# Kernel tuning notes

Hardware: AMD Instinct MI355X
Metric: run time of the kernel (lower is better)

Reference implementation:

```python
import jax, jax.numpy as jnp
import numpy as np

B, S, HID = 2, 1024, 4096
NH, NKV, HD = 32, 8, 128
GROUPS = NH // NKV  # 4
BITS = 8
SCALING = HD ** -0.5


def quantize_lastdim(x, bits=BITS):
    """Asymmetric min-max fake-quant per row of the last dim (groupsize=-1),
    matching ActQuantizer.find_params + quantize/dequantize."""
    qmax = float(2 ** bits - 1)
    xmin = jnp.minimum(jnp.min(x, axis=-1, keepdims=True), 0.0)
    xmax = jnp.maximum(jnp.max(x, axis=-1, keepdims=True), 0.0)
    rng = xmax - xmin
    scale = jnp.where(rng == 0, 1.0, rng / qmax)
    zero = jnp.round(-xmin / scale)
    q = jnp.clip(jnp.round(x / scale) + zero, 0.0, qmax)
    return (q - zero) * scale


def rotate_half(x):
    x1, x2 = jnp.split(x, 2, axis=-1)
    return jnp.concatenate([-x2, x1], axis=-1)


def setup_inputs() -> dict:
    key = jax.random.key(0)
    ks = jax.random.split(key, 5)
    hidden_states = jax.random.normal(ks[0], (B, S, HID), dtype=jnp.float32)
    w_std = 0.02
    Wq = w_std * jax.random.normal(ks[1], (NH * HD, HID), dtype=jnp.float32)
    Wk = w_std * jax.random.normal(ks[2], (NKV * HD, HID), dtype=jnp.float32)
    Wv = w_std * jax.random.normal(ks[3], (NKV * HD, HID), dtype=jnp.float32)
    Wo = w_std * jax.random.normal(ks[4], (HID, NH * HD), dtype=jnp.float32)
    # RoPE tables (theta=10000)
    inv_freq = 1.0 / (10000.0 ** (jnp.arange(0, HD, 2, dtype=jnp.float32) / HD))
    freqs = jnp.outer(jnp.arange(S, dtype=jnp.float32), inv_freq)  # [S, HD/2]
    emb = jnp.concatenate([freqs, freqs], axis=-1)  # [S, HD]
    cos = jnp.broadcast_to(jnp.cos(emb)[None], (B, S, HD)).astype(jnp.float32)
    sin = jnp.broadcast_to(jnp.sin(emb)[None], (B, S, HD)).astype(jnp.float32)
    # additive causal mask [B,1,S,S]
    causal = jnp.tril(jnp.ones((S, S), dtype=bool))
    attention_mask = jnp.where(causal, 0.0, -1e9).astype(jnp.float32)
    attention_mask = jnp.broadcast_to(attention_mask[None, None], (B, 1, S, S))
    return {"hidden_states": hidden_states, "cos": cos, "sin": sin,
            "attention_mask": attention_mask, "Wq": Wq, "Wk": Wk, "Wv": Wv, "Wo": Wo}


def reference(hidden_states, cos, sin, attention_mask, Wq, Wk, Wv, Wo):
    b, s, _ = hidden_states.shape
    # projections -> [B, H, S, D]
    q = (hidden_states @ Wq.T).reshape(b, s, NH, HD).transpose(0, 2, 1, 3)
    k = (hidden_states @ Wk.T).reshape(b, s, NKV, HD).transpose(0, 2, 1, 3)
    v = (hidden_states @ Wv.T).reshape(b, s, NKV, HD).transpose(0, 2, 1, 3)
    # RoPE (HF: unsqueeze cos/sin at head dim)
    c = cos[:, None, :, :]
    si = sin[:, None, :, :]
    q = q * c + rotate_half(q) * si
    k = k * c + rotate_half(k) * si
    # SmoothK per-channel: subtract per-channel mean over the sequence
    # (softmax-invariant outlier smoothing of K before quantization)
    k = k - jnp.mean(k, axis=2, keepdims=True)
    # activation fake-quant of Q, K (per token over head_dim)
    q = quantize_lastdim(q)
    k = quantize_lastdim(k)
    # V quantized along the sequence axis (module transposes dims 2,3 first)
    v = quantize_lastdim(v.transpose(0, 1, 3, 2)).transpose(0, 1, 3, 2)
    # GQA repeat
    k_rep = jnp.repeat(k, GROUPS, axis=1)
    v_rep = jnp.repeat(v, GROUPS, axis=1)
    scores = jnp.einsum('bhqd,bhkd->bhqk', q, k_rep) * SCALING + attention_mask
    w = jax.nn.softmax(scores.astype(jnp.float32), axis=-1).astype(q.dtype)
    # fake-quant attention weights per row (groupsize=-1, so no padding)
    w = quantize_lastdim(w)
    attn = jnp.einsum('bhqk,bhkd->bhqd', w, v_rep)
    attn = attn.transpose(0, 2, 1, 3).reshape(b, s, NH * HD)
    out = attn @ Wo.T
    return (out, w)
```

## Files before the change

kernel.cpp:

```cpp
#include <hip/hip_runtime.h>
#include <math.h>
#include <stdint.h>

typedef unsigned int u32;
typedef unsigned short u16;
typedef __bf16 bf16x8 __attribute__((ext_vector_type(8)));
typedef float f32x4 __attribute__((ext_vector_type(4)));
typedef unsigned short u16x8 __attribute__((ext_vector_type(8)));
typedef unsigned short u16x4 __attribute__((ext_vector_type(4)));

constexpr int   Bb  = 2;
constexpr int   Ss  = 1024;
constexpr int   HID = 4096;
constexpr int   NH  = 32;
constexpr int   NKV = 8;
constexpr int   HD  = 128;
constexpr float SCALING = 0.0883883476483184405501f;

enum { M_QKV = 0, M_OUT = 3 };

__device__ __forceinline__ u16 f2bf(float f) {
  u32 u = __builtin_bit_cast(u32, f);
  u = u + 0x7fffu + ((u >> 16) & 1u);
  return (u16)(u >> 16);
}

__device__ __forceinline__ void gld_lds16(const void* g, void* l) {
  __builtin_amdgcn_global_load_lds(
      (const __attribute__((address_space(1))) u32*)(uintptr_t)g,
      (__attribute__((address_space(3))) u32*)(uintptr_t)l, 16, 0, 0);
}

template <int MODE>
__global__ __launch_bounds__(512) void mfma_gemm(
    const u16* __restrict__ Abf_g,
    const u16* __restrict__ B0, const u16* __restrict__ B1,
    const u16* __restrict__ B2,
    float* __restrict__ Cf, float* __restrict__ Ck, float* __restrict__ Cv,
    int K) {
  __shared__ u16 As[3][128 * 64];
  __shared__ u16 Bs[3][256 * 64];

  const int tid = threadIdx.x;
  const int lane = tid & 63;
  const int wid = tid >> 6;
  const int wr = wid >> 2;
  const int wc = wid & 3;
  const int fr = lane & 15;
  const int fq = lane >> 4;

  const int m0 = blockIdx.y * 128;
  int nloc = 0;

  const u16* Abf = Abf_g + (size_t)m0 * K;
  const u16* Bp = nullptr;
  int which = 0;

  if (MODE == M_QKV) {
    const int j = blockIdx.x;
    if (j < 16)      { which = 0; Bp = B0 + (size_t)j * 256 * K;        nloc = j * 256; }
    else if (j < 20) { which = 1; Bp = B1 + (size_t)(j - 16) * 256 * K; nloc = (j - 16) * 256; }
    else             { which = 2; Bp = B2 + (size_t)(j - 20) * 256 * K; nloc = (j - 20) * 256; }
  } else {
    Bp = B0 + (size_t)blockIdx.x * 256 * K;
    nloc = blockIdx.x * 256;
  }

  f32x4 acc[4][4];
#pragma unroll
  for (int i = 0; i < 4; i++)
#pragma unroll
    for (int j = 0; j < 4; j++) acc[i][j] = (f32x4){0.f, 0.f, 0.f, 0.f};

  const int arow0 = wr * 64 + wc * 16;
  const int brow0 = wc * 64 + wr * 32;
  const int sub8 = lane >> 3;
  const int sl8 = lane & 7;

  auto stageA = [&](int t, int s) {
    const int ko = t * 64;
#pragma unroll
    for (int g = 0; g < 2; ++g) {
      const int r0 = arow0 + g * 8;
      const int row = r0 + sub8;
      gld_lds16(Abf + (size_t)row * K + ko + ((sl8 ^ (row & 7)) * 8),
                &As[s][r0 * 64]);
    }
  };
  auto stageB2 = [&](int t, int s, int gbase) {
    const int ko = t * 64;
#pragma unroll
    for (int g = 0; g < 2; ++g) {
      const int r0 = brow0 + (gbase + g) * 8;
      const int row = r0 + sub8;
      gld_lds16(Bp + (size_t)row * K + ko + ((sl8 ^ (row & 7)) * 8),
                &Bs[s][r0 * 64]);
    }
  };

  const int nk = K >> 6;

  stageA(0, 0); stageB2(0, 0, 0); stageB2(0, 0, 2);
  stageA(1, 1); stageB2(1, 1, 0); stageB2(1, 1, 2);
  asm volatile("s_waitcnt vmcnt(6)" ::: "memory");
  __builtin_amdgcn_sched_barrier(0);
  __builtin_amdgcn_s_barrier();

  int buf = 0, nxt = 2;
  for (int kt = 0; kt < nk; ++kt) {
    const bool st = (kt + 2 < nk);

    {
      bf16x8 av[4], bv[4];
#pragma unroll
      for (int i = 0; i < 4; ++i) {
        const int r = wr * 64 + i * 16 + fr;
        av[i] = *(const bf16x8*)&As[buf][r * 64 + ((fq ^ (r & 7)) * 8)];
      }
#pragma unroll
      for (int j = 0; j < 4; ++j) {
        const int r = wc * 64 + j * 16 + fr;
        bv[j] = *(const bf16x8*)&Bs[buf][r * 64 + ((fq ^ (r & 7)) * 8)];
      }
      if (st) { stageA(kt + 2, nxt); stageB2(kt + 2, nxt, 0); }
      __builtin_amdgcn_s_barrier();
      asm volatile("s_waitcnt lgkmcnt(0)" ::: "memory");
      __builtin_amdgcn_sched_barrier(0);
      __builtin_amdgcn_s_setprio(1);
#pragma unroll
      for (int i = 0; i < 4; i++)
#pragma unroll
        for (int j = 0; j < 4; j++)
          acc[i][j] = __builtin_amdgcn_mfma_f32_16x16x32_bf16(av[i], bv[j], acc[i][j], 0, 0, 0);
      __builtin_amdgcn_s_setprio(0);
    }

    {
      bf16x8 av[4], bv[4];
#pragma unroll
      for (int i = 0; i < 4; ++i) {
        const int r = wr * 64 + i * 16 + fr;
        av[i] = *(const bf16x8*)&As[buf][r * 64 + (((4 + fq) ^ (r & 7)) * 8)];
      }
#pragma unroll
      for (int j = 0; j < 4; ++j) {
        const int r = wc * 64 + j * 16 + fr;
        bv[j] = *(const bf16x8*)&Bs[buf][r * 64 + (((4 + fq) ^ (r & 7)) * 8)];
      }
      if (st) { stageB2(kt + 2, nxt, 2); }
      __builtin_amdgcn_s_barrier();
      asm volatile("s_waitcnt lgkmcnt(0)" ::: "memory");
      __builtin_amdgcn_sched_barrier(0);
      __builtin_amdgcn_s_setprio(1);
#pragma unroll
      for (int i = 0; i < 4; i++)
#pragma unroll
        for (int j = 0; j < 4; j++)
          acc[i][j] = __builtin_amdgcn_mfma_f32_16x16x32_bf16(av[i], bv[j], acc[i][j], 0, 0, 0);
      __builtin_amdgcn_s_setprio(0);
    }

    if (st) {
      asm volatile("s_waitcnt vmcnt(6)" ::: "memory");
    } else {
      asm volatile("s_waitcnt vmcnt(0)" ::: "memory");
    }
    __builtin_amdgcn_sched_barrier(0);
    __builtin_amdgcn_s_barrier();
    buf = (buf == 2) ? 0 : buf + 1;
    nxt = (nxt == 2) ? 0 : nxt + 1;
  }

#pragma unroll
  for (int i = 0; i < 4; i++) {
#pragma unroll
    for (int j = 0; j < 4; j++) {
      const int n = nloc + wc * 64 + j * 16 + fr;
#pragma unroll
      for (int e = 0; e < 4; e++) {
        const int m = m0 + wr * 64 + i * 16 + fq * 4 + e;
        float val = acc[i][j][e];
        if (MODE == M_QKV) {
          const int b = m >> 10, s = m & 1023, h = n >> 7, d = n & 127;
          if (which == 0)      Cf[((size_t)(b * NH + h) * Ss + s) * HD + d] = val;
          else if (which == 1) Ck[((size_t)(b * NKV + h) * Ss + s) * HD + d] = val;
          else                 Cv[((size_t)(b * NKV + h) * HD + d) * Ss + s] = val;
        } else {
          Cf[(size_t)m * HID + n] = val;
        }
      }
    }
  }
}

__global__ __launch_bounds__(256) void fused_attn(
    const u16* __restrict__ qb,
    const u16* __restrict__ kb,
    const u16* __restrict__ vTb,
    float* __restrict__ wout,
    u16* __restrict__ attnb) {
  __shared__ u16 Ks[64 * 128];
  __shared__ u16 Vs[128 * 64];
  __shared__ u16 plds[4][16 * 64];
  __shared__ float scl_l[4][16];

  const int a = 15 - (int)(blockIdx.x >> 6);
  const int bh = blockIdx.x & 63;
  const int b = bh >> 5, h = bh & 31;
  const int kv = h >> 2;
  const int tid = threadIdx.x;
  const int lane = tid & 63;
  const int wq = tid >> 6;
  const int fr = lane & 15, fq = lane >> 4;

  const int nt = a + 1;
  const int Q0 = a * 64;
  const int qw0 = Q0 + wq * 16;

  const u16* Kb = kb + (size_t)(b * NKV + kv) * Ss * HD;
  const u16* Vb = vTb + (size_t)(b * NKV + kv) * HD * Ss;
  float* wrow = wout + (size_t)bh * Ss * Ss;

  if (a < 15) {
    const int base = 64 * nt;
    const int n4 = 16 * (15 - a);
#pragma unroll
    for (int r0 = 0; r0 < 4; ++r0) {
      const int row = Q0 + r0 * 16 + (tid >> 4);
      float4* wp = (float4*)&wrow[(size_t)row * Ss + base];
      for (int c = tid & 15; c < n4; c += 16) wp[c] = float4{0.f, 0.f, 0.f, 0.f};
    }
  }

  bf16x8 qf[4];
#pragma unroll
  for (int kk = 0; kk < 4; kk++)
    qf[kk] = *(const bf16x8*)&qb[((size_t)bh * Ss + qw0 + fr) * HD + kk * 32 + fq * 8];

  float m[4], l[4];
#pragma unroll
  for (int i = 0; i < 4; i++) { m[i] = -1e30f; l[i] = 0.f; }

  for (int t = 0; t < nt; ++t) {
    __syncthreads();
#pragma unroll
    for (int c = 0; c < 4; ++c) {
      const int idx0 = (c * 4 + wq) * 64;
      const int idx = idx0 + lane;
      const int row = idx >> 4, sl = idx & 15;
      const int slot = sl ^ (row & 15);
      gld_lds16(Kb + (size_t)(t * 64 + row) * HD + slot * 8, &Ks[idx0 * 8]);
    }
    __syncthreads();

    f32x4 sa[4];
#pragma unroll
    for (int jn = 0; jn < 4; jn++) sa[jn] = (f32x4){0.f, 0.f, 0.f, 0.f};
#pragma unroll
    for (int kk = 0; kk < 4; ++kk) {
      bf16x8 kfv[4];
#pragma unroll
      for (int jn = 0; jn < 4; ++jn) {
        const int row = jn * 16 + fr;
        kfv[jn] = *(const bf16x8*)&Ks[row * 128 + (((kk * 4 + fq) ^ fr) * 8)];
      }
#pragma unroll
      for (int jn = 0; jn < 4; ++jn)
        sa[jn] = __builtin_amdgcn_mfma_f32_16x16x32_bf16(qf[kk], kfv[jn], sa[jn], 0, 0, 0);
    }

    const bool diag = (t == a);
#pragma unroll
    for (int e = 0; e < 4; ++e) {
      const int qrow = qw0 + fq * 4 + e;
      float sv[4];
      float rmax = -1e30f;
#pragma unroll
      for (int jn = 0; jn < 4; ++jn) {
        float s = sa[jn][e] * SCALING;
        if (diag && (t * 64 + jn * 16 + fr > qrow)) s = -1e30f;
        sv[jn] = s;
        rmax = fmaxf(rmax, s);
      }
#pragma unroll
      for (int o = 1; o < 16; o <<= 1) rmax = fmaxf(rmax, __shfl_xor(rmax, o));
      const float mn = fmaxf(m[e], rmax);
      const float cc = __expf(m[e] - mn);
      float rs = __expf(sv[0] - mn) + __expf(sv[1] - mn) +
                 __expf(sv[2] - mn) + __expf(sv[3] - mn);
#pragma unroll
      for (int o = 1; o < 16; o <<= 1) rs += __shfl_xor(rs, o);
      l[e] = l[e] * cc + rs;
      m[e] = mn;
    }
  }

  float scl[4];
#pragma unroll
  for (int e = 0; e < 4; e++) scl[e] = 1.f / (255.f * l[e]);
  if (fr == 0) {
#pragma unroll
    for (int e = 0; e < 4; e++) scl_l[wq][fq * 4 + e] = scl[e];
  }

  f32x4 acc2[8];
#pragma unroll
  for (int j = 0; j < 8; j++) acc2[j] = (f32x4){0.f, 0.f, 0.f, 0.f};

  u16* pl = &plds[wq][0];
  const int wrrow = lane >> 2, wrq = lane & 3;
  const float sclr = scl_l[wq][wrrow];

  for (int t = 0; t < nt; ++t) {
    __syncthreads();
#pragma unroll
    for (int c = 0; c < 4; ++c) {
      const int idx0 = (c * 4 + wq) * 64;
      const int idx = idx0 + lane;
      {
        const int row = idx >> 4, sl = idx & 15;
        const int slot = sl ^ (row & 15);
        gld_lds16(Kb + (size_t)(t * 64 + row) * HD + slot * 8, &Ks[idx0 * 8]);
      }
      {
        const int d = idx >> 3, sl = idx & 7;
        const int slot = sl ^ (d & 7);
        gld_lds16(Vb + (size_t)d * Ss + t * 64 + slot * 8, &Vs[idx0 * 8]);
      }
    }
    __syncthreads();

    f32x4 sa[4];
#pragma unroll
    for (int jn = 0; jn < 4; jn++) sa[jn] = (f32x4){0.f, 0.f, 0.f, 0.f};
#pragma unroll
    for (int kk = 0; kk < 4; ++kk) {
      bf16x8 kfv[4];
#pragma unroll
      for (int jn = 0; jn < 4; ++jn) {
        const int row = jn * 16 + fr;
        kfv[jn] = *(const bf16x8*)&Ks[row * 128 + (((kk * 4 + fq) ^ fr) * 8)];
      }
#pragma unroll
      for (int jn = 0; jn < 4; ++jn)
        sa[jn] = __builtin_amdgcn_mfma_f32_16x16x32_bf16(qf[kk], kfv[jn], sa[jn], 0, 0, 0);
    }

    const bool diag = (t == a);
#pragma unroll
    for (int e = 0; e < 4; ++e) {
      const int qrow = qw0 + fq * 4 + e;
      const int r16 = fq * 4 + e;
#pragma unroll
      for (int jn = 0; jn < 4; ++jn) {
        const int kc = t * 64 + jn * 16 + fr;
        float qv = 0.f;
        if (!diag || kc <= qrow)
          qv = rintf(fminf(255.f * __expf(sa[jn][e] * SCALING - m[e]), 255.f));
        const int col = jn * 16 + fr;
        const int byte = r16 * 128 + (((col >> 3) ^ (r16 & 7)) * 16) + (col & 7) * 2;
        *(u16*)((char*)pl + byte) = f2bf(qv);
      }
    }

    {
      const int s0 = (2 * wrq) ^ (wrrow & 7);
      const int s1 = (2 * wrq + 1) ^ (wrrow & 7);
      bf16x8 p0 = *(const bf16x8*)((char*)pl + wrrow * 128 + s0 * 16);
      bf16x8 p1 = *(const bf16x8*)((char*)pl + wrrow * 128 + s1 * 16);
      float* wp = &wrow[(size_t)(qw0 + wrrow) * Ss + t * 64 + wrq * 16];
      float4 o0, o1, o2, o3;
      o0.x = (float)p0[0] * sclr; o0.y = (float)p0[1] * sclr;
      o0.z = (float)p0[2] * sclr; o0.w = (float)p0[3] * sclr;
      o1.x = (float)p0[4] * sclr; o1.y = (float)p0[5] * sclr;
      o1.z = (float)p0[6] * sclr; o1.w = (float)p0[7] * sclr;
      o2.x = (float)p1[0] * sclr; o2.y = (float)p1[1] * sclr;
      o2.z = (float)p1[2] * sclr; o2.w = (float)p1[3] * sclr;
      o3.x = (float)p1[4] * sclr; o3.y = (float)p1[5] * sclr;
      o3.z = (float)p1[6] * sclr; o3.w = (float)p1[7] * sclr;
      ((float4*)wp)[0] = o0; ((float4*)wp)[1] = o1;
      ((float4*)wp)[2] = o2; ((float4*)wp)[3] = o3;
    }

#pragma unroll
    for (int kk2 = 0; kk2 < 2; ++kk2) {
      const bf16x8 pa = *(const bf16x8*)((char*)pl + fr * 128 + (((kk2 * 4 + fq) ^ (fr & 7)) * 16));
#pragma unroll
      for (int jn2 = 0; jn2 < 8; ++jn2) {
        const int d = jn2 * 16 + fr;
        const bf16x8 vb = *(const bf16x8*)&Vs[d * 64 + (((kk2 * 4 + fq) ^ (d & 7)) * 8)];
        acc2[jn2] = __builtin_amdgcn_mfma_f32_16x16x32_bf16(pa, vb, acc2[jn2], 0, 0, 0);
      }
    }
  }

#pragma unroll
  for (int e = 0; e < 4; ++e) {
    const int qrow = qw0 + fq * 4 + e;
#pragma unroll
    for (int jn2 = 0; jn2 < 8; ++jn2)
      attnb[((size_t)b * Ss + qrow) * HID + h * HD + jn2 * 16 + fr] =
          f2bf(acc2[jn2][e] * scl[e]);
  }
}

constexpr int CB_HS = Bb * Ss * HID / 2048;
constexpr int CB_WQ = NH * HD * HID / 2048;
constexpr int CB_WK = NKV * HD * HID / 2048;
constexpr int CB_WV = CB_WK;
constexpr int CB_WO = HID * NH * HD / 2048;

__global__ __launch_bounds__(256) void convert_all(
    const float* __restrict__ hs, const float* __restrict__ wq,
    const float* __restrict__ wk, const float* __restrict__ wv,
    const float* __restrict__ wo,
    u16* __restrict__ hsb, u16* __restrict__ wqb, u16* __restrict__ wkb,
    u16* __restrict__ wvb, u16* __restrict__ wob) {
  const int bid = blockIdx.x;
  const float* src;
  u16* dst;
  int base;
  if (bid < CB_HS) { src = hs; dst = hsb; base = 0; }
  else if (bid < CB_HS + CB_WQ) { src = wq; dst = wqb; base = CB_HS; }
  else if (bid < CB_HS + CB_WQ + CB_WK) { src = wk; dst = wkb; base = CB_HS + CB_WQ; }
  else if (bid < CB_HS + CB_WQ + CB_WK + CB_WV) { src = wv; dst = wvb; base = CB_HS + CB_WQ + CB_WK; }
  else { src = wo; dst = wob; base = CB_HS + CB_WQ + CB_WK + CB_WV; }
  const int i = (bid - base) * 256 + threadIdx.x;
  float4 a = ((const float4*)src)[2 * i];
  float4 b = ((const float4*)src)[2 * i + 1];
  u16x8 t;
  t[0] = f2bf(a.x); t[1] = f2bf(a.y); t[2] = f2bf(a.z); t[3] = f2bf(a.w);
  t[4] = f2bf(b.x); t[5] = f2bf(b.y); t[6] = f2bf(b.z); t[7] = f2bf(b.w);
  ((u16x8*)dst)[i] = t;
}

__global__ __launch_bounds__(256) void rope_quant_q(const float* __restrict__ q,
                                                    u16* __restrict__ qb,
                                                    const float* __restrict__ cs,
                                                    const float* __restrict__ sn) {
  const int row = blockIdx.x * 4 + (threadIdx.x >> 6);
  const int lane = threadIdx.x & 63;
  const int s = row & (Ss - 1);
  const int b = row >> 15;
  const float* p = q + (size_t)row * HD;
  const float* cp = cs + ((size_t)b * Ss + s) * HD;
  const float* sp = sn + ((size_t)b * Ss + s) * HD;
  float x1 = p[lane], x2 = p[lane + 64];
  float r1 = x1 * cp[lane] - x2 * sp[lane];
  float r2 = x2 * cp[lane + 64] + x1 * sp[lane + 64];
  float mn = fminf(0.f, fminf(r1, r2));
  float mx = fmaxf(0.f, fmaxf(r1, r2));
#pragma unroll
  for (int o = 32; o; o >>= 1) {
    mn = fminf(mn, __shfl_xor(mn, o));
    mx = fmaxf(mx, __shfl_xor(mx, o));
  }
  float rng = mx - mn;
  float scale = (rng == 0.f) ? 1.f : rng / 255.f;
  float zero = rintf(-mn / scale);
  float q1 = fminf(fmaxf(rintf(r1 / scale) + zero, 0.f), 255.f);
  float q2 = fminf(fmaxf(rintf(r2 / scale) + zero, 0.f), 255.f);
  qb[(size_t)row * HD + lane] = f2bf((q1 - zero) * scale);
  qb[(size_t)row * HD + lane + 64] = f2bf((q2 - zero) * scale);
}

__global__ __launch_bounds__(256) void rope_k(float* __restrict__ k,
                                              const float* __restrict__ cs,
                                              const float* __restrict__ sn) {
  const int row = blockIdx.x * 4 + (threadIdx.x >> 6);
  const int lane = threadIdx.x & 63;
  const int s = row & (Ss - 1);
  const int b = row >> 13;
  float* p = k + (size_t)row * HD;
  const float* cp = cs + ((size_t)b * Ss + s) * HD;
  const float* sp = sn + ((size_t)b * Ss + s) * HD;
  float x1 = p[lane], x2 = p[lane + 64];
  float r1 = x1 * cp[lane] - x2 * sp[lane];
  float r2 = x2 * cp[lane + 64] + x1 * sp[lane + 64];
  p[lane] = r1;
  p[lane + 64] = r2;
}

__global__ __launch_bounds__(1024) void kmean_kernel(const float* __restrict__ k,
                                                     float* __restrict__ kmean) {
  const int bh = blockIdx.x;
  const int d = threadIdx.x & 127;
  const int sl = threadIdx.x >> 7;
  const float* p = k + (size_t)bh * Ss * HD;
  float sum = 0.f;
  for (int s = sl; s < Ss; s += 8) sum += p[(size_t)s * HD + d];
  __shared__ float lds[8][128];
  lds[sl][d] = sum;
  __syncthreads();
  if (threadIdx.x < 128) {
    float t = 0.f;
#pragma unroll
    for (int i = 0; i < 8; i++) t += lds[i][threadIdx.x];
    kmean[bh * HD + threadIdx.x] = t * (1.f / 1024.f);
  }
}

__global__ __launch_bounds__(256) void k_subquant(const float* __restrict__ k,
                                                  u16* __restrict__ kb,
                                                  const float* __restrict__ kmean) {
  const int row = blockIdx.x * 4 + (threadIdx.x >> 6);
  const int lane = threadIdx.x & 63;
  const int bh = row >> 10;
  const float* p = k + (size_t)row * HD;
  float x1 = p[lane] - kmean[bh * HD + lane];
  float x2 = p[lane + 64] - kmean[bh * HD + lane + 64];
  float mn = fminf(0.f, fminf(x1, x2));
  float mx = fmaxf(0.f, fmaxf(x1, x2));
#pragma unroll
  for (int o = 32; o; o >>= 1) {
    mn = fminf(mn, __shfl_xor(mn, o));
    mx = fmaxf(mx, __shfl_xor(mx, o));
  }
  float rng = mx - mn;
  float scale = (rng == 0.f) ? 1.f : rng / 255.f;
  float zero = rintf(-mn / scale);
  float q1 = fminf(fmaxf(rintf(x1 / scale) + zero, 0.f), 255.f);
  float q2 = fminf(fmaxf(rintf(x2 / scale) + zero, 0.f), 255.f);
  kb[(size_t)row * HD + lane] = f2bf((q1 - zero) * scale);
  kb[(size_t)row * HD + lane + 64] = f2bf((q2 - zero) * scale);
}

__global__ __launch_bounds__(256) void vquant(const float* __restrict__ vT,
                                              u16* __restrict__ vTb) {
  const float* p = vT + (size_t)blockIdx.x * Ss;
  const int t = threadIdx.x;
  float4 x = ((const float4*)p)[t];
  float mn = fminf(0.f, fminf(fminf(x.x, x.y), fminf(x.z, x.w)));
  float mx = fmaxf(0.f, fmaxf(fmaxf(x.x, x.y), fmaxf(x.z, x.w)));
#pragma unroll
  for (int o = 32; o; o >>= 1) {
    mn = fminf(mn, __shfl_xor(mn, o));
    mx = fmaxf(mx, __shfl_xor(mx, o));
  }
  __shared__ float smn[4], smx[4];
  const int wid = t >> 6, lane = t & 63;
  if (lane == 0) { smn[wid] = mn; smx[wid] = mx; }
  __syncthreads();
  mn = fminf(fminf(smn[0], smn[1]), fminf(smn[2], smn[3]));
  mx = fmaxf(fmaxf(smx[0], smx[1]), fmaxf(smx[2], smx[3]));
  float rng = mx - mn;
  float scale = (rng == 0.f) ? 1.f : rng / 255.f;
  float zero = rintf(-mn / scale);
  u16x4 o4;
  o4[0] = f2bf((fminf(fmaxf(rintf(x.x / scale) + zero, 0.f), 255.f) - zero) * scale);
  o4[1] = f2bf((fminf(fmaxf(rintf(x.y / scale) + zero, 0.f), 255.f) - zero) * scale);
  o4[2] = f2bf((fminf(fmaxf(rintf(x.z / scale) + zero, 0.f), 255.f) - zero) * scale);
  o4[3] = f2bf((fminf(fmaxf(rintf(x.w / scale) + zero, 0.f), 255.f) - zero) * scale);
  ((u16x4*)vTb)[(size_t)blockIdx.x * 256 + t] = o4;
}

extern "C" void kernel_launch(void* const* d_in, const int* in_sizes, int n_in,
                              void* d_out, int out_size, void* d_ws, size_t ws_size,
                              hipStream_t stream) {
  const float* hs = (const float*)d_in[0];
  const float* cosp = (const float*)d_in[1];
  const float* sinp = (const float*)d_in[2];
  const float* Wq = (const float*)d_in[4];
  const float* Wk = (const float*)d_in[5];
  const float* Wv = (const float*)d_in[6];
  const float* Wo = (const float*)d_in[7];

  float* out = (float*)d_out;
  float* wout = out + (size_t)Bb * Ss * HID;

  char* wsp = (char*)d_ws;
  auto alloc = [&](size_t bytes) {
    char* p = wsp;
    wsp += (bytes + 255) & ~(size_t)255;
    return p;
  };
  float* q     = (float*)alloc((size_t)Bb * NH * Ss * HD * 4);
  float* k     = (float*)alloc((size_t)Bb * NKV * Ss * HD * 4);
  float* vT    = (float*)alloc((size_t)Bb * NKV * Ss * HD * 4);
  float* kmean = (float*)alloc((size_t)Bb * NKV * HD * 4);
  u16* hsb = (u16*)alloc((size_t)Bb * Ss * HID * 2);
  u16* qb  = (u16*)alloc((size_t)Bb * NH * Ss * HD * 2);
  u16* kb  = (u16*)alloc((size_t)Bb * NKV * Ss * HD * 2);
  u16* vTb = (u16*)alloc((size_t)Bb * NKV * Ss * HD * 2);
  u16* Wqb = (u16*)alloc((size_t)NH * HD * HID * 2);
  u16* Wkb = (u16*)alloc((size_t)NKV * HD * HID * 2);
  u16* Wvb = (u16*)alloc((size_t)NKV * HD * HID * 2);
  u16* Wob = (u16*)alloc((size_t)HID * NH * HD * 2);
  u16* attnb = (u16*)q;

  convert_all<<<CB_HS + CB_WQ + CB_WK + CB_WV + CB_WO, 256, 0, stream>>>(
      hs, Wq, Wk, Wv, Wo, hsb, Wqb, Wkb, Wvb, Wob);

  mfma_gemm<M_QKV><<<dim3(24, 16), 512, 0, stream>>>(
      hsb, Wqb, Wkb, Wvb, q, k, vT, HID);

  rope_quant_q<<<(Bb * NH * Ss) / 4, 256, 0, stream>>>(q, qb, cosp, sinp);
  rope_k<<<(Bb * NKV * Ss) / 4, 256, 0, stream>>>(k, cosp, sinp);
  kmean_kernel<<<Bb * NKV, 1024, 0, stream>>>(k, kmean);
  k_subquant<<<(Bb * NKV * Ss) / 4, 256, 0, stream>>>(k, kb, kmean);
  vquant<<<Bb * NKV * HD, 256, 0, stream>>>(vT, vTb);

  fused_attn<<<dim3(1024), 256, 0, stream>>>(qb, kb, vTb, wout, attnb);

  mfma_gemm<M_OUT><<<dim3(16, 16), 512, 0, stream>>>(
      attnb, Wob, nullptr, nullptr, out, nullptr, nullptr, HID);
}
```

Baseline: 442.0 us.

## Double-buffer attention tiles, enlarge attention blocks, remap GEMM grid, fuse post-projection kernels

The attention kernel now handles 128 query rows per 512-thread block and double-buffers K/V tiles in LDS, prefetching the next tile while the current one is computed. The P staging buffer reuses the K buffer. The GEMMs use a 1D grid with an XCD-aware block remap for better L2 locality, and V is stored with float4 writes. The RoPE-Q/quant, RoPE-K and V-quant kernels are merged into one launch to cut launch overhead. The extra barriers and the larger LDS footprint may limit occupancy.

Measured after the change: 480.0 us. 1.09x slower.

```diff
diff --git a/kernel.cpp b/kernel.cpp
--- a/kernel.cpp
+++ b/kernel.cpp
@@ -49,7 +49,14 @@
   const int fr = lane & 15;
   const int fq = lane >> 4;
 
-  const int m0 = blockIdx.y * 128;
+  constexpr int GX = (MODE == M_QKV) ? 24 : 16;
+  constexpr int CPX = (MODE == M_QKV) ? 48 : 32;
+  const int bid = blockIdx.x;
+  const int wg = (bid & 7) * CPX + (bid >> 3);
+  const int bx = wg % GX;
+  const int by = wg / GX;
+
+  const int m0 = by * 128;
   int nloc = 0;
 
   const u16* Abf = Abf_g + (size_t)m0 * K;
@@ -57,13 +64,12 @@
   int which = 0;
 
   if (MODE == M_QKV) {
-    const int j = blockIdx.x;
-    if (j < 16)      { which = 0; Bp = B0 + (size_t)j * 256 * K;        nloc = j * 256; }
-    else if (j < 20) { which = 1; Bp = B1 + (size_t)(j - 16) * 256 * K; nloc = (j - 16) * 256; }
-    else             { which = 2; Bp = B2 + (size_t)(j - 20) * 256 * K; nloc = (j - 20) * 256; }
+    if (bx < 16)      { which = 0; Bp = B0 + (size_t)bx * 256 * K;        nloc = bx * 256; }
+    else if (bx < 20) { which = 1; Bp = B1 + (size_t)(bx - 16) * 256 * K; nloc = (bx - 16) * 256; }
+    else              { which = 2; Bp = B2 + (size_t)(bx - 20) * 256 * K; nloc = (bx - 20) * 256; }
   } else {
-    Bp = B0 + (size_t)blockIdx.x * 256 * K;
-    nloc = blockIdx.x * 256;
+    Bp = B0 + (size_t)bx * 256 * K;
+    nloc = bx * 256;
   }
 
   f32x4 acc[4][4];
@@ -176,35 +182,40 @@
 #pragma unroll
     for (int j = 0; j < 4; j++) {
       const int n = nloc + wc * 64 + j * 16 + fr;
-#pragma unroll
-      for (int e = 0; e < 4; e++) {
-        const int m = m0 + wr * 64 + i * 16 + fq * 4 + e;
-        float val = acc[i][j][e];
-        if (MODE == M_QKV) {
-          const int b = m >> 10, s = m & 1023, h = n >> 7, d = n & 127;
-          if (which == 0)      Cf[((size_t)(b * NH + h) * Ss + s) * HD + d] = val;
-          else if (which == 1) Ck[((size_t)(b * NKV + h) * Ss + s) * HD + d] = val;
-          else                 Cv[((size_t)(b * NKV + h) * HD + d) * Ss + s] = val;
-        } else {
-          Cf[(size_t)m * HID + n] = val;
+      const int mb = m0 + wr * 64 + i * 16 + fq * 4;
+      if (MODE == M_QKV && which == 2) {
+        const int b = mb >> 10, s = mb & 1023, h = n >> 7, d = n & 127;
+        float4 v4 = {acc[i][j][0], acc[i][j][1], acc[i][j][2], acc[i][j][3]};
+        *(float4*)&Cv[((size_t)(b * NKV + h) * HD + d) * Ss + s] = v4;
+      } else {
+#pragma unroll
+        for (int e = 0; e < 4; e++) {
+          const int m = mb + e;
+          float val = acc[i][j][e];
+          if (MODE == M_QKV) {
+            const int b = m >> 10, s = m & 1023, h = n >> 7, d = n & 127;
+            if (which == 0) Cf[((size_t)(b * NH + h) * Ss + s) * HD + d] = val;
+            else            Ck[((size_t)(b * NKV + h) * Ss + s) * HD + d] = val;
+          } else {
+            Cf[(size_t)m * HID + n] = val;
+          }
         }
       }
     }
   }
 }
 
-__global__ __launch_bounds__(256) void fused_attn(
+__global__ __launch_bounds__(512, 4) void fused_attn(
     const u16* __restrict__ qb,
     const u16* __restrict__ kb,
     const u16* __restrict__ vTb,
     float* __restrict__ wout,
     u16* __restrict__ attnb) {
-  __shared__ u16 Ks[64 * 128];
-  __shared__ u16 Vs[128 * 64];
-  __shared__ u16 plds[4][16 * 64];
-  __shared__ float scl_l[4][16];
-
-  const int a = 15 - (int)(blockIdx.x >> 6);
+  __shared__ u16 Ks[2][64 * 128];
+  __shared__ u16 Vs[2][128 * 64];
+  __shared__ float scl_l[8][16];
+
+  const int a = 7 - (int)(blockIdx.x >> 6);
   const int bh = blockIdx.x & 63;
   const int b = bh >> 5, h = bh & 31;
   const int kv = h >> 2;
@@ -213,24 +224,43 @@
   const int wq = tid >> 6;
   const int fr = lane & 15, fq = lane >> 4;
 
-  const int nt = a + 1;
-  const int Q0 = a * 64;
+  const int nt = 2 * a + 2;
+  const int Q0 = a * 128;
   const int qw0 = Q0 + wq * 16;
+  const int dband = qw0 >> 6;
 
   const u16* Kb = kb + (size_t)(b * NKV + kv) * Ss * HD;
   const u16* Vb = vTb + (size_t)(b * NKV + kv) * HD * Ss;
   float* wrow = wout + (size_t)bh * Ss * Ss;
 
-  if (a < 15) {
+  if (a < 7) {
     const int base = 64 * nt;
-    const int n4 = 16 * (15 - a);
-#pragma unroll
-    for (int r0 = 0; r0 < 4; ++r0) {
-      const int row = Q0 + r0 * 16 + (tid >> 4);
-      float4* wp = (float4*)&wrow[(size_t)row * Ss + base];
-      for (int c = tid & 15; c < n4; c += 16) wp[c] = float4{0.f, 0.f, 0.f, 0.f};
-    }
-  }
+    const int n4 = (Ss - base) >> 2;
+    const int row = Q0 + (tid >> 2);
+    float4* wp = (float4*)&wrow[(size_t)row * Ss + base];
+    for (int c = tid & 3; c < n4; c += 4) wp[c] = float4{0.f, 0.f, 0.f, 0.f};
+  }
+
+  auto stageK = [&](int t, int s) {
+#pragma unroll
+    for (int g = 0; g < 2; ++g) {
+      const int c = wq * 2 + g;
+      const int idx = c * 64 + lane;
+      const int row = idx >> 4, sl = idx & 15;
+      const int slot = sl ^ (row & 15);
+      gld_lds16(Kb + (size_t)(t * 64 + row) * HD + slot * 8, &Ks[s][c * 512]);
+    }
+  };
+  auto stageV = [&](int t, int s) {
+#pragma unroll
+    for (int g = 0; g < 2; ++g) {
+      const int c = wq * 2 + g;
+      const int idx = c * 64 + lane;
+      const int d = idx >> 3, sl = idx & 7;
+      const int slot = sl ^ (d & 7);
+      gld_lds16(Vb + (size_t)d * Ss + t * 64 + slot * 8, &Vs[s][c * 512]);
+    }
+  };
 
   bf16x8 qf[4];
 #pragma unroll
@@ -241,17 +271,17 @@
 #pragma unroll
   for (int i = 0; i < 4; i++) { m[i] = -1e30f; l[i] = 0.f; }
 
+  stageK(0, 0);
   for (int t = 0; t < nt; ++t) {
-    __syncthreads();
-#pragma unroll
-    for (int c = 0; c < 4; ++c) {
-      const int idx0 = (c * 4 + wq) * 64;
-      const int idx = idx0 + lane;
-      const int row = idx >> 4, sl = idx & 15;
-      const int slot = sl ^ (row & 15);
-      gld_lds16(Kb + (size_t)(t * 64 + row) * HD + slot * 8, &Ks[idx0 * 8]);
-    }
-    __syncthreads();
+    if (t + 1 < nt) {
+      stageK(t + 1, (t + 1) & 1);
+      asm volatile("s_waitcnt vmcnt(2)" ::: "memory");
+    } else {
+      asm volatile("s_waitcnt vmcnt(0)" ::: "memory");
+    }
+    __builtin_amdgcn_sched_barrier(0);
+    __builtin_amdgcn_s_barrier();
+    const u16* Kt = &Ks[t & 1][0];
 
     f32x4 sa[4];
 #pragma unroll
@@ -262,14 +292,14 @@
 #pragma unroll
       for (int jn = 0; jn < 4; ++jn) {
         const int row = jn * 16 + fr;
-        kfv[jn] = *(const bf16x8*)&Ks[row * 128 + (((kk * 4 + fq) ^ fr) * 8)];
+        kfv[jn] = *(const bf16x8*)&Kt[row * 128 + (((kk * 4 + fq) ^ fr) * 8)];
       }
 #pragma unroll
       for (int jn = 0; jn < 4; ++jn)
         sa[jn] = __builtin_amdgcn_mfma_f32_16x16x32_bf16(qf[kk], kfv[jn], sa[jn], 0, 0, 0);
     }
 
-    const bool diag = (t == a);
+    const bool diag = (t >= dband);
 #pragma unroll
     for (int e = 0; e < 4; ++e) {
       const int qrow = qw0 + fq * 4 + e;
@@ -293,6 +323,7 @@
       l[e] = l[e] * cc + rs;
       m[e] = mn;
     }
+    __builtin_amdgcn_s_barrier();
   }
 
   float scl[4];
@@ -307,28 +338,24 @@
 #pragma unroll
   for (int j = 0; j < 8; j++) acc2[j] = (f32x4){0.f, 0.f, 0.f, 0.f};
 
-  u16* pl = &plds[wq][0];
   const int wrrow = lane >> 2, wrq = lane & 3;
   const float sclr = scl_l[wq][wrrow];
 
+  stageK(0, 0);
+  stageV(0, 0);
   for (int t = 0; t < nt; ++t) {
-    __syncthreads();
-#pragma unroll
-    for (int c = 0; c < 4; ++c) {
-      const int idx0 = (c * 4 + wq) * 64;
-      const int idx = idx0 + lane;
-      {
-        const int row = idx >> 4, sl = idx & 15;
-        const int slot = sl ^ (row & 15);
-        gld_lds16(Kb + (size_t)(t * 64 + row) * HD + slot * 8, &Ks[idx0 * 8]);
-      }
-      {
-        const int d = idx >> 3, sl = idx & 7;
-        const int slot = sl ^ (d & 7);
-        gld_lds16(Vb + (size_t)d * Ss + t * 64 + slot * 8, &Vs[idx0 * 8]);
-      }
-    }
-    __syncthreads();
+    if (t + 1 < nt) {
+      stageK(t + 1, (t + 1) & 1);
+      stageV(t + 1, (t + 1) & 1);
+      asm volatile("s_waitcnt vmcnt(4)" ::: "memory");
+    } else {
+      asm volatile("s_waitcnt vmcnt(0)" ::: "memory");
+    }
+    __builtin_amdgcn_sched_barrier(0);
+    __builtin_amdgcn_s_barrier();
+    const u16* Kt = &Ks[t & 1][0];
+    const u16* Vt = &Vs[t & 1][0];
+    u16* pl = &Ks[t & 1][wq * 1024];
 
     f32x4 sa[4];
 #pragma unroll
@@ -339,14 +366,15 @@
 #pragma unroll
       for (int jn = 0; jn < 4; ++jn) {
         const int row = jn * 16 + fr;
-        kfv[jn] = *(const bf16x8*)&Ks[row * 128 + (((kk * 4 + fq) ^ fr) * 8)];
+        kfv[jn] = *(const bf16x8*)&Kt[row * 128 + (((kk * 4 + fq) ^ fr) * 8)];
       }
 #pragma unroll
       for (int jn = 0; jn < 4; ++jn)
         sa[jn] = __builtin_amdgcn_mfma_f32_16x16x32_bf16(qf[kk], kfv[jn], sa[jn], 0, 0, 0);
     }
-
-    const bool diag = (t == a);
+    __builtin_amdgcn_s_barrier();
+
+    const bool diag = (t >= dband);
 #pragma unroll
     for (int e = 0; e < 4; ++e) {
       const int qrow = qw0 + fq * 4 + e;
@@ -388,10 +416,11 @@
 #pragma unroll
       for (int jn2 = 0; jn2 < 8; ++jn2) {
         const int d = jn2 * 16 + fr;
-        const bf16x8 vb = *(const bf16x8*)&Vs[d * 64 + (((kk2 * 4 + fq) ^ (d & 7)) * 8)];
+        const bf16x8 vb = *(const bf16x8*)&Vt[d * 64 + (((kk2 * 4 + fq) ^ (d & 7)) * 8)];
         acc2[jn2] = __builtin_amdgcn_mfma_f32_16x16x32_bf16(pa, vb, acc2[jn2], 0, 0, 0);
       }
     }
+    __builtin_amdgcn_s_barrier();
   }
 
 #pragma unroll
@@ -434,51 +463,82 @@
   ((u16x8*)dst)[i] = t;
 }
 
-__global__ __launch_bounds__(256) void rope_quant_q(const float* __restrict__ q,
-                                                    u16* __restrict__ qb,
-                                                    const float* __restrict__ cs,
-                                                    const float* __restrict__ sn) {
-  const int row = blockIdx.x * 4 + (threadIdx.x >> 6);
-  const int lane = threadIdx.x & 63;
-  const int s = row & (Ss - 1);
-  const int b = row >> 15;
-  const float* p = q + (size_t)row * HD;
-  const float* cp = cs + ((size_t)b * Ss + s) * HD;
-  const float* sp = sn + ((size_t)b * Ss + s) * HD;
-  float x1 = p[lane], x2 = p[lane + 64];
-  float r1 = x1 * cp[lane] - x2 * sp[lane];
-  float r2 = x2 * cp[lane + 64] + x1 * sp[lane + 64];
-  float mn = fminf(0.f, fminf(r1, r2));
-  float mx = fmaxf(0.f, fmaxf(r1, r2));
-#pragma unroll
-  for (int o = 32; o; o >>= 1) {
-    mn = fminf(mn, __shfl_xor(mn, o));
-    mx = fmaxf(mx, __shfl_xor(mx, o));
-  }
-  float rng = mx - mn;
-  float scale = (rng == 0.f) ? 1.f : rng / 255.f;
-  float zero = rintf(-mn / scale);
-  float q1 = fminf(fmaxf(rintf(r1 / scale) + zero, 0.f), 255.f);
-  float q2 = fminf(fmaxf(rintf(r2 / scale) + zero, 0.f), 255.f);
-  qb[(size_t)row * HD + lane] = f2bf((q1 - zero) * scale);
-  qb[(size_t)row * HD + lane + 64] = f2bf((q2 - zero) * scale);
-}
-
-__global__ __launch_bounds__(256) void rope_k(float* __restrict__ k,
-                                              const float* __restrict__ cs,
-                                              const float* __restrict__ sn) {
-  const int row = blockIdx.x * 4 + (threadIdx.x >> 6);
-  const int lane = threadIdx.x & 63;
-  const int s = row & (Ss - 1);
-  const int b = row >> 13;
-  float* p = k + (size_t)row * HD;
-  const float* cp = cs + ((size_t)b * Ss + s) * HD;
-  const float* sp = sn + ((size_t)b * Ss + s) * HD;
-  float x1 = p[lane], x2 = p[lane + 64];
-  float r1 = x1 * cp[lane] - x2 * sp[lane];
-  float r2 = x2 * cp[lane + 64] + x1 * sp[lane + 64];
-  p[lane] = r1;
-  p[lane + 64] = r2;
+constexpr int PQ_Q = (Bb * NH * Ss) / 4;
+constexpr int PQ_K = (Bb * NKV * Ss) / 4;
+constexpr int PQ_V = Bb * NKV * HD;
+
+__global__ __launch_bounds__(256) void postq(
+    const float* __restrict__ q, u16* __restrict__ qb,
+    float* __restrict__ k,
+    const float* __restrict__ vT, u16* __restrict__ vTb,
+    const float* __restrict__ cs, const float* __restrict__ sn) {
+  const int bid = blockIdx.x;
+  if (bid < PQ_Q) {
+    const int row = bid * 4 + (threadIdx.x >> 6);
+    const int lane = threadIdx.x & 63;
+    const int s = row & (Ss - 1);
+    const int b = row >> 15;
+    const float* p = q + (size_t)row * HD;
+    const float* cp = cs + ((size_t)b * Ss + s) * HD;
+    const float* sp = sn + ((size_t)b * Ss + s) * HD;
+    float x1 = p[lane], x2 = p[lane + 64];
+    float r1 = x1 * cp[lane] - x2 * sp[lane];
+    float r2 = x2 * cp[lane + 64] + x1 * sp[lane + 64];
+    float mn = fminf(0.f, fminf(r1, r2));
+    float mx = fmaxf(0.f, fmaxf(r1, r2));
+#pragma unroll
+    for (int o = 32; o; o >>= 1) {
+      mn = fminf(mn, __shfl_xor(mn, o));
+      mx = fmaxf(mx, __shfl_xor(mx, o));
+    }
+    float rng = mx - mn;
+    float scale = (rng == 0.f) ? 1.f : rng / 255.f;
+    float zero = rintf(-mn / scale);
+    float q1 = fminf(fmaxf(rintf(r1 / scale) + zero, 0.f), 255.f);
+    float q2 = fminf(fmaxf(rintf(r2 / scale) + zero, 0.f), 255.f);
+    qb[(size_t)row * HD + lane] = f2bf((q1 - zero) * scale);
+    qb[(size_t)row * HD + lane + 64] = f2bf((q2 - zero) * scale);
+  } else if (bid < PQ_Q + PQ_K) {
+    const int row = (bid - PQ_Q) * 4 + (threadIdx.x >> 6);
+    const int lane = threadIdx.x & 63;
+    const int s = row & (Ss - 1);
+    const int b = row >> 13;
+    float* p = k + (size_t)row * HD;
+    const float* cp = cs + ((size_t)b * Ss + s) * HD;
+    const float* sp = sn + ((size_t)b * Ss + s) * HD;
+    float x1 = p[lane], x2 = p[lane + 64];
+    float r1 = x1 * cp[lane] - x2 * sp[lane];
+    float r2 = x2 * cp[lane + 64] + x1 * sp[lane + 64];
+    p[lane] = r1;
+    p[lane + 64] = r2;
+  } else {
+    const int vb = bid - PQ_Q - PQ_K;
+    const float* p = vT + (size_t)vb * Ss;
+    const int t = threadIdx.x;
+    float4 x = ((const float4*)p)[t];
+    float mn = fminf(0.f, fminf(fminf(x.x, x.y), fminf(x.z, x.w)));
+    float mx = fmaxf(0.f, fmaxf(fmaxf(x.x, x.y), fmaxf(x.z, x.w)));
+#pragma unroll
+    for (int o = 32; o; o >>= 1) {
+      mn = fminf(mn, __shfl_xor(mn, o));
+      mx = fmaxf(mx, __shfl_xor(mx, o));
+    }
+    __shared__ float smn[4], smx[4];
+    const int wid = t >> 6, lane = t & 63;
+    if (lane == 0) { smn[wid] = mn; smx[wid] = mx; }
+    __syncthreads();
+    mn = fminf(fminf(smn[0], smn[1]), fminf(smn[2], smn[3]));
+    mx = fmaxf(fmaxf(smx[0], smx[1]), fmaxf(smx[2], smx[3]));
+    float rng = mx - mn;
+    float scale = (rng == 0.f) ? 1.f : rng / 255.f;
+    float zero = rintf(-mn / scale);
+    u16x4 o4;
+    o4[0] = f2bf((fminf(fmaxf(rintf(x.x / scale) + zero, 0.f), 255.f) - zero) * scale);
+    o4[1] = f2bf((fminf(fmaxf(rintf(x.y / scale) + zero, 0.f), 255.f) - zero) * scale);
+    o4[2] = f2bf((fminf(fmaxf(rintf(x.z / scale) + zero, 0.f), 255.f) - zero) * scale);
+    o4[3] = f2bf((fminf(fmaxf(rintf(x.w / scale) + zero, 0.f), 255.f) - zero) * scale);
+    ((u16x4*)vTb)[(size_t)vb * 256 + t] = o4;
+  }
 }
 
 __global__ __launch_bounds__(1024) void kmean_kernel(const float* __restrict__ k,
@@ -523,35 +583,6 @@
   float q2 = fminf(fmaxf(rintf(x2 / scale) + zero, 0.f), 255.f);
   kb[(size_t)row * HD + lane] = f2bf((q1 - zero) * scale);
   kb[(size_t)row * HD + lane + 64] = f2bf((q2 - zero) * scale);
-}
-
-__global__ __launch_bounds__(256) void vquant(const float* __restrict__ vT,
-                                              u16* __restrict__ vTb) {
-  const float* p = vT + (size_t)blockIdx.x * Ss;
-  const int t = threadIdx.x;
-  float4 x = ((const float4*)p)[t];
-  float mn = fminf(0.f, fminf(fminf(x.x, x.y), fminf(x.z, x.w)));
-  float mx = fmaxf(0.f, fmaxf(fmaxf(x.x, x.y), fmaxf(x.z, x.w)));
-#pragma unroll
-  for (int o = 32; o; o >>= 1) {
-    mn = fminf(mn, __shfl_xor(mn, o));
-    mx = fmaxf(mx, __shfl_xor(mx, o));
-  }
-  __shared__ float smn[4], smx[4];
-  const int wid = t >> 6, lane = t & 63;
-  if (lane == 0) { smn[wid] = mn; smx[wid] = mx; }
-  __syncthreads();
-  mn = fminf(fminf(smn[0], smn[1]), fminf(smn[2], smn[3]));
-  mx = fmaxf(fmaxf(smx[0], smx[1]), fmaxf(smx[2], smx[3]));
-  float rng = mx - mn;
-  float scale = (rng == 0.f) ? 1.f : rng / 255.f;
-  float zero = rintf(-mn / scale);
-  u16x4 o4;
-  o4[0] = f2bf((fminf(fmaxf(rintf(x.x / scale) + zero, 0.f), 255.f) - zero) * scale);
-  o4[1] = f2bf((fminf(fmaxf(rintf(x.y / scale) + zero, 0.f), 255.f) - zero) * scale);
-  o4[2] = f2bf((fminf(fmaxf(rintf(x.z / scale) + zero, 0.f), 255.f) - zero) * scale);
-  o4[3] = f2bf((fminf(fmaxf(rintf(x.w / scale) + zero, 0.f), 255.f) - zero) * scale);
-  ((u16x4*)vTb)[(size_t)blockIdx.x * 256 + t] = o4;
 }
 
 extern "C" void kernel_launch(void* const* d_in, const int* in_sizes, int n_in,
@@ -591,17 +622,15 @@
   convert_all<<<CB_HS + CB_WQ + CB_WK + CB_WV + CB_WO, 256, 0, stream>>>(
       hs, Wq, Wk, Wv, Wo, hsb, Wqb, Wkb, Wvb, Wob);
 
-  mfma_gemm<M_QKV><<<dim3(24, 16), 512, 0, stream>>>(
+  mfma_gemm<M_QKV><<<dim3(384), 512, 0, stream>>>(
       hsb, Wqb, Wkb, Wvb, q, k, vT, HID);
 
-  rope_quant_q<<<(Bb * NH * Ss) / 4, 256, 0, stream>>>(q, qb, cosp, sinp);
-  rope_k<<<(Bb * NKV * Ss) / 4, 256, 0, stream>>>(k, cosp, sinp);
+  postq<<<PQ_Q + PQ_K + PQ_V, 256, 0, stream>>>(q, qb, k, vT, vTb, cosp, sinp);
   kmean_kernel<<<Bb * NKV, 1024, 0, stream>>>(k, kmean);
   k_subquant<<<(Bb * NKV * Ss) / 4, 256, 0, stream>>>(k, kb, kmean);
-  vquant<<<Bb * NKV * HD, 256, 0, stream>>>(vT, vTb);
-
-  fused_attn<<<dim3(1024), 256, 0, stream>>>(qb, kb, vTb, wout, attnb);
-
-  mfma_gemm<M_OUT><<<dim3(16, 16), 512, 0, stream>>>(
+
+  fused_attn<<<dim3(512), 512, 0, stream>>>(qb, kb, vTb, wout, attnb);
+
+  mfma_gemm<M_OUT><<<dim3(256), 512, 0, stream>>>(
       attnb, Wob, nullptr, nullptr, out, nullptr, nullptr, HID);
 }
```
